# Performance work log

Measured on AMD Instinct MI355X. Metric: run time of the kernel, lower is better.

## Reference

```python
import jax, jax.numpy as jnp
import numpy as np


def _quant(x):
    # Per-tensor dynamic uint8 quantization to produce LUT row/col indices.
    # (The CUDA kernel's exact requant scheme is not in the source; this is the
    # assumed scheme: scale so max |x| -> 255, round, clip to [0,255].)
    s = 255.0 / jnp.maximum(jnp.max(jnp.abs(x)), jnp.float32(1e-6))
    return jnp.clip(jnp.round(x * s), 0, 255).astype(jnp.int32)


def _lut_conv(x, w, b, lut):
    # CustomAnyConv2d: stride=1, padding=(2,2), kernel 5x5.
    O, Cin, kh, kw = w.shape
    # im2col patches: (B, Cin*kh*kw, H, W), feature ordering matches w.reshape(O, -1)
    patches = jax.lax.conv_general_dilated_patches(
        x, (kh, kw), (1, 1), ((2, 2), (2, 2)))
    B, K, H, W = patches.shape
    pi = _quant(patches).reshape(B, K, H * W)            # (B,K,P)
    wi = _quant(w.reshape(O, K))                          # (O,K)
    vals = lut[pi[:, None, :, :], wi[None, :, :, None]]   # (B,O,K,P) gather
    out = vals.sum(axis=2).reshape(B, O, H, W)            # accumulate LUT products
    return out + b[None, :, None, None]


def _lut_dense(x, w, b, lut):
    # CustomAnyDense: out[h, o] = sum_k LUT[x[h,k], w[o,k]] + b[o]
    xi = _quant(x)                                        # (B,K)
    wi = _quant(w)                                        # (O,K)
    vals = lut[xi[:, None, :], wi[None, :, :]]            # (B,O,K)
    return vals.sum(axis=2) + b


def _maxpool2(x, pad=0):
    return jax.lax.reduce_window(
        x, -jnp.inf, jax.lax.max,
        (1, 1, 2, 2), (1, 1, 2, 2),
        ((0, 0), (0, 0), (pad, pad), (pad, pad)))


def setup_inputs() -> dict:
    key = jax.random.key(0)
    ks = jax.random.split(key, 11)
    B = 32
    x = jax.random.uniform(ks[0], (B, 1, 28, 28), jnp.float32)
    ij = np.arange(256)
    # Approximate-multiplier LUT: high byte of exact 8x8-bit product (uint8-valued).
    lut = jnp.asarray(((ij[:, None] * ij[None, :]) >> 8).astype(np.float32))
    return {
        "x": x,
        "lut": lut,
        "w1": jax.random.uniform(ks[1], (16, 1, 5, 5), jnp.float32),
        "b1": jax.random.normal(ks[2], (16,), jnp.float32) * 0.01,
        "w2": jax.random.uniform(ks[3], (32, 16, 5, 5), jnp.float32),
        "b2": jax.random.normal(ks[4], (32,), jnp.float32) * 0.01,
        "w3": jax.random.uniform(ks[5], (64, 32, 5, 5), jnp.float32),
        "b3": jax.random.normal(ks[6], (64,), jnp.float32) * 0.01,
        "fw1": jax.random.uniform(ks[7], (256, 1024), jnp.float32),
        "fb1": jax.random.normal(ks[8], (256,), jnp.float32) * 0.01,
        "fw2": jax.random.uniform(ks[9], (10, 256), jnp.float32),
        "fb2": jax.random.normal(ks[10], (10,), jnp.float32) * 0.01,
    }


def reference(x, lut, w1, b1, w2, b2, w3, b3, fw1, fb1, fw2, fb2):
    h = jax.nn.relu(_lut_conv(x, w1, b1, lut))
    h = _maxpool2(h)                     # (B,16,14,14)
    h = jax.nn.relu(_lut_conv(h, w2, b2, lut))
    h = _maxpool2(h)                     # (B,32,7,7)
    h = jax.nn.relu(_lut_conv(h, w3, b3, lut))
    h = _maxpool2(h, pad=1)              # (B,64,4,4)
    h = h.reshape(h.shape[0], -1)        # (B,1024)
    h = jax.nn.relu(_lut_dense(h, fw1, fb1, lut))
    h = _lut_dense(h, fw2, fb2, lut)     # (B,10)
    return jax.nn.log_softmax(h, axis=1)
```

## Files before the change

### kernel.cpp

```cpp
#include <hip/hip_runtime.h>
#include <math.h>

typedef unsigned int  u32;
typedef unsigned short u16;
typedef unsigned short u16x2 __attribute__((ext_vector_type(2)));

#define MAGIC 0x5A17D0E5u

#define O_XFLAGS 256
#define O_FLAGS  1024
#define O_A1     4096
#define O_A2     405504
#define O_A3     606208
#define O_A4     737280

__device__ __forceinline__ float blk_max(float v, float* red) {
  int t = threadIdx.x;
  __syncthreads();
  red[t] = v;
  __syncthreads();
#pragma unroll
  for (int s = 128; s > 0; s >>= 1) {
    if (t < s) red[t] = fmaxf(red[t], red[t + s]);
    __syncthreads();
  }
  return red[0];
}

__device__ __forceinline__ void amax_f(float* slot, float v) {
  atomicMax((int*)slot, (int)__float_as_uint(v));
}

__device__ __forceinline__ u16 quant1(float v, float s) {
  float q = rintf(v * s);
  q = fminf(fmaxf(q, 0.0f), 255.0f);
  return (u16)q;
}

__device__ __forceinline__ void mac_u32(u32& acc, u32 a, u32 w) {
  u16x2 av = __builtin_bit_cast(u16x2, a);
  u16x2 wv = __builtin_bit_cast(u16x2, w);
  u16x2 p  = av * wv;
  acc += (__builtin_bit_cast(u32, p) >> 8) & 0x00FF00FFu;
}
__device__ __forceinline__ void mac4(u32& acc, uint4 a, uint4 w) {
  mac_u32(acc, a.x, w.x); mac_u32(acc, a.y, w.y);
  mac_u32(acc, a.z, w.z); mac_u32(acc, a.w, w.w);
}

__device__ __forceinline__ float fmax4(float4 v) {
  return fmaxf(fmaxf(fabsf(v.x), fabsf(v.y)), fmaxf(fabsf(v.z), fabsf(v.w)));
}

__global__ __launch_bounds__(256, 2) void k_conv1(
    const float* __restrict__ x, const float* __restrict__ w1, const float* __restrict__ b1,
    const float* __restrict__ w2, const float* __restrict__ w3,
    const float* __restrict__ fw1, const float* __restrict__ fw2,
    float* __restrict__ a1, float* wsf, u32* xflags) {
  __shared__ float sxf[1024];
  __shared__ unsigned char sx[1024];
  __shared__ u16 sw[64];
  __shared__ float red[256];
  const int t = threadIdx.x, bid = blockIdx.x;

  if (bid >= 256) {
    int sb = bid - 256;
    if (sb < 16) {
      const float4* x4 = (const float4*)x;
      float m = 0.f;
      for (int i = sb * 256 + t; i < 6272; i += 16 * 256) m = fmaxf(m, fmax4(x4[i]));
      m = blk_max(m, red);
      if (t == 0) {
        amax_f(wsf + 0, m);
        __hip_atomic_store(&xflags[sb], MAGIC, __ATOMIC_RELEASE, __HIP_MEMORY_SCOPE_AGENT);
      }
      return;
    }
    sb -= 16;
    const float* p; int n4, base, nb, slot;
    if (sb < 2)       { p = w2;  n4 = 3200;  base = sb;      nb = 2;  slot = 2; }
    else if (sb < 10) { p = w3;  n4 = 12800; base = sb - 2;  nb = 8;  slot = 3; }
    else if (sb < 58) { p = fw1; n4 = 65536; base = sb - 10; nb = 48; slot = 4; }
    else              { p = fw2; n4 = 640;   base = 0;       nb = 1;  slot = 5; }
    const float4* p4 = (const float4*)p;
    float m = 0.f;
    for (int i = base * 256 + t; i < n4; i += nb * 256) m = fmaxf(m, fmax4(p4[i]));
    m = blk_max(m, red);
    if (t == 0) amax_f(wsf + slot, m);
    return;
  }

  int b = bid >> 3, op = bid & 7;
  float m = 0.f;
  if (t < 100) m = fmax4(((const float4*)w1)[t]);
  float w1max = blk_max(m, red);
  float sw1s = 255.0f / fmaxf(w1max, 1e-6f);
  for (int i = t; i < 1024; i += 256) sxf[i] = 0.f;
  __syncthreads();
  for (int i = t; i < 784; i += 256) {
    int y = i / 28, xx = i - y * 28;
    sxf[(y + 2) * 32 + xx + 2] = x[b * 784 + i];
  }
  if (t < 50) sw[t] = quant1(w1[op * 50 + t], sw1s);
  {
    int it = 0, ok = 0;
    do {
      u32 f = (t < 16) ? __hip_atomic_load(&xflags[t], __ATOMIC_RELAXED, __HIP_MEMORY_SCOPE_AGENT)
                       : MAGIC;
      ok = __syncthreads_and(f == MAGIC);
      if (!ok) __builtin_amdgcn_s_sleep(1);
    } while (!ok && ++it < 2000000);
    __threadfence();
  }
  float s0 = 255.0f / fmaxf(wsf[0], 1e-6f);
  for (int i = t; i < 1024; i += 256) sx[i] = (unsigned char)quant1(sxf[i], s0);
  __syncthreads();
  float lm = 0.f;
  if (t < 196) {
    int py = t / 14, px = t - py * 14;
#pragma unroll
    for (int ol = 0; ol < 2; ++ol) {
      int oc = op * 2 + ol;
      int best = -2147483647;
#pragma unroll
      for (int dy = 0; dy < 2; ++dy)
#pragma unroll
        for (int dx = 0; dx < 2; ++dx) {
          int cy = 2 * py + dy, cx = 2 * px + dx;
          int acc = 0;
#pragma unroll
          for (int kh = 0; kh < 5; ++kh) {
            const unsigned char* xp = sx + (cy + kh) * 32 + cx;
#pragma unroll
            for (int kw = 0; kw < 5; ++kw)
              acc += ((int)xp[kw] * (int)sw[ol * 25 + kh * 5 + kw]) >> 8;
          }
          best = max(best, acc);
        }
      float v = fmaxf(0.f, (float)best + b1[oc]);
      a1[b * 3136 + t * 16 + oc] = v;
      lm = fmaxf(lm, v);
    }
  }
  lm = blk_max(lm, red);
  if (t == 0) amax_f(wsf + 6, lm);
}

__global__ __launch_bounds__(256) void k_conv2(
    const float* __restrict__ a1, const float* __restrict__ w2, const float* __restrict__ b2,
    float* __restrict__ a2, float* wsf) {
  __shared__ __align__(16) u16 sa[324 * 16];
  __shared__ __align__(16) u16 sw[800];
  __shared__ int sconv[196];
  __shared__ float red[256];
  const int t = threadIdx.x, bid = blockIdx.x;
  int b = bid >> 4, og = bid & 15;
  float s1 = 255.0f / fmaxf(wsf[6], 1e-6f);
  float sw2 = 255.0f / fmaxf(wsf[2], 1e-6f);
  u32* sz = (u32*)sa;
  for (int i = t; i < 2592; i += 256) sz[i] = 0;
  __syncthreads();
  for (int i = t; i < 3136; i += 256) {
    int px = i >> 4, c = i & 15;
    int y = px / 14, xx = px - y * 14;
    sa[((y + 2) * 18 + xx + 2) * 16 + c] = quant1(a1[b * 3136 + i], s1);
  }
  for (int i = t; i < 800; i += 256) {
    int ol = i / 400, r = i - ol * 400, c = r / 25, tp = r - c * 25;
    sw[ol * 400 + tp * 16 + c] = quant1(w2[(og * 2 + ol) * 400 + c * 25 + tp], sw2);
  }
  __syncthreads();
  int h = t & 1, pxb = t >> 1;
  float lm = 0.f;
  for (int ol = 0; ol < 2; ++ol) {
    int oc = og * 2 + ol;
    const uint4* wq = (const uint4*)(sw + ol * 400);
#pragma unroll
    for (int rep = 0; rep < 2; ++rep) {
      int px = pxb + rep * 128;
      if (px < 196) {
        int y = px / 14, xx = px - y * 14;
        u32 acc = 0;
#pragma unroll
        for (int kh = 0; kh < 5; ++kh)
#pragma unroll
          for (int kw = 0; kw < 5; ++kw) {
            int row = (y + kh) * 18 + (xx + kw);
            uint4 av = *(const uint4*)(sa + row * 16 + h * 8);
            mac4(acc, av, wq[(kh * 5 + kw) * 2 + h]);
          }
        int ai = (int)((acc & 0xFFFFu) + (acc >> 16));
        ai += __shfl_down(ai, 1, 2);
        if (h == 0) sconv[px] = ai;
      }
    }
    __syncthreads();
    if (t < 49) {
      int py = t / 7, px = t - py * 7;
      int mm = sconv[(2 * py) * 14 + 2 * px];
      mm = max(mm, sconv[(2 * py) * 14 + 2 * px + 1]);
      mm = max(mm, sconv[(2 * py + 1) * 14 + 2 * px]);
      mm = max(mm, sconv[(2 * py + 1) * 14 + 2 * px + 1]);
      float v = fmaxf(0.f, (float)mm + b2[oc]);
      a2[b * 1568 + t * 32 + oc] = v;
      lm = fmaxf(lm, v);
    }
    __syncthreads();
  }
  lm = blk_max(lm, red);
  if (t == 0) amax_f(wsf + 7, lm);
}

__global__ __launch_bounds__(256) void k_conv3(
    const float* __restrict__ a2, const float* __restrict__ w3, const float* __restrict__ b3,
    float* __restrict__ a3, float* wsf) {
  __shared__ __align__(16) u16 sa[121 * 40];
  __shared__ __align__(16) u16 sw[4 * 800];
  __shared__ float red[256];
  const int t = threadIdx.x, bid = blockIdx.x;
  int b = bid >> 4, og = bid & 15;
  float s2 = 255.0f / fmaxf(wsf[7], 1e-6f);
  float sw3 = 255.0f / fmaxf(wsf[3], 1e-6f);
  u32* sz = (u32*)sa;
  for (int i = t; i < 2420; i += 256) sz[i] = 0;
  __syncthreads();
  for (int i = t; i < 1568; i += 256) {
    int px = i >> 5, c = i & 31;
    int y = px / 7, xx = px - y * 7;
    sa[((y + 2) * 11 + xx + 2) * 40 + c] = quant1(a2[b * 1568 + i], s2);
  }
  for (int i = t; i < 3200; i += 256) {
    int ol = i / 800, r = i - ol * 800, c = r / 25, tp = r - c * 25;
    sw[ol * 800 + tp * 32 + c] = quant1(w3[(og * 4 + ol) * 800 + c * 25 + tp], sw3);
  }
  __syncthreads();
  int q = t & 3, pos = t >> 2;
  int dydx = pos & 3, r = pos >> 2;
  int py = r >> 2, px = r & 3;
  int cy = 2 * py - 1 + (dydx >> 1), cx = 2 * px - 1 + (dydx & 1);
  bool valid = (cy >= 0 && cy < 7 && cx >= 0 && cx < 7);
  float lm = 0.f;
  for (int ol = 0; ol < 4; ++ol) {
    int oc = og * 4 + ol;
    int ai = 0;
    if (valid) {
      u32 acc = 0;
#pragma unroll
      for (int kh = 0; kh < 5; ++kh)
#pragma unroll
        for (int kw = 0; kw < 5; ++kw) {
          int row = (cy + kh) * 11 + (cx + kw);
          uint4 av = *(const uint4*)(sa + row * 40 + q * 8);
          uint4 wv = *(const uint4*)(sw + ol * 800 + (kh * 5 + kw) * 32 + q * 8);
          mac4(acc, av, wv);
        }
      ai = (int)((acc & 0xFFFFu) + (acc >> 16));
    }
    ai += __shfl_down(ai, 2, 4);
    ai += __shfl_down(ai, 1, 4);
    int val = valid ? ai : -(1 << 30);
    int mm = max(val, __shfl_down(val, 4, 16));
    mm = max(mm, __shfl_down(mm, 8, 16));
    if ((t & 15) == 0) {
      float v = fmaxf(0.f, (float)mm + b3[oc]);
      a3[b * 1024 + oc * 16 + r] = v;
      lm = fmaxf(lm, v);
    }
  }
  lm = blk_max(lm, red);
  if (t == 0) amax_f(wsf + 8, lm);
}

__global__ __launch_bounds__(256) void k_dense12(
    const float* __restrict__ a3f, const float* __restrict__ fw1, const float* __restrict__ fb1,
    const float* __restrict__ fw2, const float* __restrict__ fb2,
    float* __restrict__ a4, float* __restrict__ out, float* wsf, u32* flags) {
  __shared__ union {
    struct { u16 sh[1024]; } p;
    struct { u16 sh2[32 * 264]; u16 qw[2560]; float zb[320]; } w;
  } sm;
  __shared__ float red[256];
  const int t = threadIdx.x, bid = blockIdx.x;

  if (bid < 512) {
    int b = bid >> 4, og = bid & 15;
    float s3 = 255.0f / fmaxf(wsf[8], 1e-6f);
    float sws = 255.0f / fmaxf(wsf[4], 1e-6f);
    for (int i = t; i < 1024; i += 256)
      sm.p.sh[i] = quant1(a3f[b * 1024 + i], s3);
    __syncthreads();
    int ol = t >> 4, ks = t & 15;
    int o = og * 16 + ol;
    const float4* wf = (const float4*)(fw1 + o * 1024);
    const uint4* hp = (const uint4*)sm.p.sh;
    u32 acc = 0;
#pragma unroll
    for (int j = 0; j < 8; ++j) {
      int e = j * 16 + ks;
      float4 f0 = wf[e * 2], f1 = wf[e * 2 + 1];
      uint4 wv;
      wv.x = (u32)quant1(f0.x, sws) | ((u32)quant1(f0.y, sws) << 16);
      wv.y = (u32)quant1(f0.z, sws) | ((u32)quant1(f0.w, sws) << 16);
      wv.z = (u32)quant1(f1.x, sws) | ((u32)quant1(f1.y, sws) << 16);
      wv.w = (u32)quant1(f1.z, sws) | ((u32)quant1(f1.w, sws) << 16);
      mac4(acc, hp[e], wv);
    }
    int ai = (int)((acc & 0xFFFFu) + (acc >> 16));
#pragma unroll
    for (int d = 8; d > 0; d >>= 1)
      ai += __shfl_down(ai, d, 16);
    float lm = 0.f;
    if (ks == 0) {
      float v = fmaxf(0.f, (float)ai + fb1[o]);
      a4[b * 256 + o] = v;
      lm = v;
    }
    lm = blk_max(lm, red);
    if (t == 0) amax_f(wsf + 9, lm);
    __syncthreads();
    if (t == 0)
      __hip_atomic_store(&flags[bid], MAGIC, __ATOMIC_RELEASE, __HIP_MEMORY_SCOPE_AGENT);
    return;
  }

  {
    long it = 0;
    int ok = 0;
    do {
      u32 f1 = __hip_atomic_load(&flags[t],       __ATOMIC_RELAXED, __HIP_MEMORY_SCOPE_AGENT);
      u32 f2 = __hip_atomic_load(&flags[t + 256], __ATOMIC_RELAXED, __HIP_MEMORY_SCOPE_AGENT);
      ok = __syncthreads_and((f1 == MAGIC) && (f2 == MAGIC));
      if (!ok) __builtin_amdgcn_s_sleep(1);
    } while (!ok && ++it < 4000000);
    __threadfence();
  }
  float s4 = 255.0f / fmaxf(wsf[9], 1e-6f);
  float s5 = 255.0f / fmaxf(wsf[5], 1e-6f);
  for (int i = t; i < 8192; i += 256) {
    int b = i >> 8, k = i & 255;
    sm.w.sh2[b * 264 + k] = quant1(a4[i], s4);
  }
  for (int i = t; i < 2560; i += 256) sm.w.qw[i] = quant1(fw2[i], s5);
  __syncthreads();
  for (int task = t; task < 320; task += 256) {
    int b = task / 10, o = task - b * 10;
    const uint4* wp = (const uint4*)(sm.w.qw + o * 256);
    const uint4* hp = (const uint4*)(sm.w.sh2 + b * 264);
    u32 acc = 0;
#pragma unroll
    for (int j = 0; j < 32; ++j)
      mac4(acc, hp[j], wp[j]);
    sm.w.zb[task] = (float)((acc & 0xFFFFu) + (acc >> 16)) + fb2[o];
  }
  __syncthreads();
  for (int task = t; task < 320; task += 256) {
    int b = task / 10;
    const float* z = sm.w.zb + b * 10;
    float m = z[0];
#pragma unroll
    for (int j = 1; j < 10; ++j) m = fmaxf(m, z[j]);
    float se = 0.f;
#pragma unroll
    for (int j = 0; j < 10; ++j) se += expf(z[j] - m);
    out[task] = sm.w.zb[task] - (m + logf(se));
  }
}

extern "C" void kernel_launch(void* const* d_in, const int* in_sizes, int n_in,
                              void* d_out, int out_size, void* d_ws, size_t ws_size,
                              hipStream_t stream) {
  const float* x   = (const float*)d_in[0];
  const float* w1  = (const float*)d_in[2];
  const float* b1  = (const float*)d_in[3];
  const float* w2  = (const float*)d_in[4];
  const float* b2  = (const float*)d_in[5];
  const float* w3  = (const float*)d_in[6];
  const float* b3  = (const float*)d_in[7];
  const float* fw1 = (const float*)d_in[8];
  const float* fb1 = (const float*)d_in[9];
  const float* fw2 = (const float*)d_in[10];
  const float* fb2 = (const float*)d_in[11];
  float* out = (float*)d_out;
  unsigned char* ws8 = (unsigned char*)d_ws;
  float* wsf = (float*)d_ws;
  u32* xflags = (u32*)(ws8 + O_XFLAGS);
  u32* flags  = (u32*)(ws8 + O_FLAGS);
  float* A1 = (float*)(ws8 + O_A1);
  float* A2 = (float*)(ws8 + O_A2);
  float* A3 = (float*)(ws8 + O_A3);
  float* A4 = (float*)(ws8 + O_A4);

  k_conv1  <<<331, 256, 0, stream>>>(x, w1, b1, w2, w3, fw1, fw2, A1, wsf, xflags);
  k_conv2  <<<512, 256, 0, stream>>>(A1, w2, b2, A2, wsf);
  k_conv3  <<<512, 256, 0, stream>>>(A2, w3, b3, A3, wsf);
  k_dense12<<<513, 256, 0, stream>>>(A3, fw1, fb1, fw2, fb2, A4, out, wsf, flags);
}
```

Before: 158.5 us.

## Replace inter-block spin-wait flags with redundant reductions and a separate dense2 launch

Conv1 no longer waits on flag blocks that compute the global input max. Every conv block now recomputes the full input abs-max itself, quantizes straight into byte shared memory, and the 2-launch-bound hint is dropped. The fused dense kernel, which spun on 512 flags before its final block ran, is split into two kernels. Dense2 now uses 32 small blocks, one per batch row, instead of a single block. This removes spin-wait latency and the serial tail block, at the cost of redundant global reads of x in each block and one more kernel launch.

```diff
diff --git a/kernel.cpp b/kernel.cpp
--- a/kernel.cpp
+++ b/kernel.cpp
@@ -5,10 +5,6 @@
 typedef unsigned short u16;
 typedef unsigned short u16x2 __attribute__((ext_vector_type(2)));
 
-#define MAGIC 0x5A17D0E5u
-
-#define O_XFLAGS 256
-#define O_FLAGS  1024
 #define O_A1     4096
 #define O_A2     405504
 #define O_A3     606208
@@ -52,12 +48,11 @@
   return fmaxf(fmaxf(fabsf(v.x), fabsf(v.y)), fmaxf(fabsf(v.z), fabsf(v.w)));
 }
 
-__global__ __launch_bounds__(256, 2) void k_conv1(
+__global__ __launch_bounds__(256) void k_conv1(
     const float* __restrict__ x, const float* __restrict__ w1, const float* __restrict__ b1,
     const float* __restrict__ w2, const float* __restrict__ w3,
     const float* __restrict__ fw1, const float* __restrict__ fw2,
-    float* __restrict__ a1, float* wsf, u32* xflags) {
-  __shared__ float sxf[1024];
+    float* __restrict__ a1, float* wsf) {
   __shared__ unsigned char sx[1024];
   __shared__ u16 sw[64];
   __shared__ float red[256];
@@ -65,18 +60,6 @@
 
   if (bid >= 256) {
     int sb = bid - 256;
-    if (sb < 16) {
-      const float4* x4 = (const float4*)x;
-      float m = 0.f;
-      for (int i = sb * 256 + t; i < 6272; i += 16 * 256) m = fmaxf(m, fmax4(x4[i]));
-      m = blk_max(m, red);
-      if (t == 0) {
-        amax_f(wsf + 0, m);
-        __hip_atomic_store(&xflags[sb], MAGIC, __ATOMIC_RELEASE, __HIP_MEMORY_SCOPE_AGENT);
-      }
-      return;
-    }
-    sb -= 16;
     const float* p; int n4, base, nb, slot;
     if (sb < 2)       { p = w2;  n4 = 3200;  base = sb;      nb = 2;  slot = 2; }
     else if (sb < 10) { p = w3;  n4 = 12800; base = sb - 2;  nb = 8;  slot = 3; }
@@ -92,28 +75,23 @@
 
   int b = bid >> 3, op = bid & 7;
   float m = 0.f;
+  const float4* x4 = (const float4*)x;
+  for (int i = t; i < 6272; i += 256) m = fmaxf(m, fmax4(x4[i]));
+  float xmax = blk_max(m, red);
+  m = 0.f;
   if (t < 100) m = fmax4(((const float4*)w1)[t]);
   float w1max = blk_max(m, red);
-  float sw1s = 255.0f / fmaxf(w1max, 1e-6f);
-  for (int i = t; i < 1024; i += 256) sxf[i] = 0.f;
+  float s0  = 255.0f / fmaxf(xmax, 1e-6f);
+  float sw1 = 255.0f / fmaxf(w1max, 1e-6f);
+
+  u32* sxz = (u32*)sx;
+  for (int i = t; i < 256; i += 256) sxz[i] = 0;
   __syncthreads();
   for (int i = t; i < 784; i += 256) {
     int y = i / 28, xx = i - y * 28;
-    sxf[(y + 2) * 32 + xx + 2] = x[b * 784 + i];
-  }
-  if (t < 50) sw[t] = quant1(w1[op * 50 + t], sw1s);
-  {
-    int it = 0, ok = 0;
-    do {
-      u32 f = (t < 16) ? __hip_atomic_load(&xflags[t], __ATOMIC_RELAXED, __HIP_MEMORY_SCOPE_AGENT)
-                       : MAGIC;
-      ok = __syncthreads_and(f == MAGIC);
-      if (!ok) __builtin_amdgcn_s_sleep(1);
-    } while (!ok && ++it < 2000000);
-    __threadfence();
-  }
-  float s0 = 255.0f / fmaxf(wsf[0], 1e-6f);
-  for (int i = t; i < 1024; i += 256) sx[i] = (unsigned char)quant1(sxf[i], s0);
+    sx[(y + 2) * 32 + xx + 2] = (unsigned char)quant1(x[b * 784 + i], s0);
+  }
+  if (t < 50) sw[t] = quant1(w1[op * 50 + t], sw1);
   __syncthreads();
   float lm = 0.f;
   if (t < 196) {
@@ -271,32 +249,68 @@
   if (t == 0) amax_f(wsf + 8, lm);
 }
 
-__global__ __launch_bounds__(256) void k_dense12(
+__global__ __launch_bounds__(256) void k_dense1(
     const float* __restrict__ a3f, const float* __restrict__ fw1, const float* __restrict__ fb1,
-    const float* __restrict__ fw2, const float* __restrict__ fb2,
-    float* __restrict__ a4, float* __restrict__ out, float* wsf, u32* flags) {
-  __shared__ union {
-    struct { u16 sh[1024]; } p;
-    struct { u16 sh2[32 * 264]; u16 qw[2560]; float zb[320]; } w;
-  } sm;
+    float* __restrict__ a4, float* wsf) {
+  __shared__ __align__(16) u16 sh[1024];
   __shared__ float red[256];
   const int t = threadIdx.x, bid = blockIdx.x;
-
-  if (bid < 512) {
-    int b = bid >> 4, og = bid & 15;
-    float s3 = 255.0f / fmaxf(wsf[8], 1e-6f);
-    float sws = 255.0f / fmaxf(wsf[4], 1e-6f);
-    for (int i = t; i < 1024; i += 256)
-      sm.p.sh[i] = quant1(a3f[b * 1024 + i], s3);
-    __syncthreads();
-    int ol = t >> 4, ks = t & 15;
-    int o = og * 16 + ol;
-    const float4* wf = (const float4*)(fw1 + o * 1024);
-    const uint4* hp = (const uint4*)sm.p.sh;
+  int b = bid >> 4, og = bid & 15;
+  float s3 = 255.0f / fmaxf(wsf[8], 1e-6f);
+  float sws = 255.0f / fmaxf(wsf[4], 1e-6f);
+  for (int i = t; i < 1024; i += 256)
+    sh[i] = quant1(a3f[b * 1024 + i], s3);
+  __syncthreads();
+  int ol = t >> 4, ks = t & 15;
+  int o = og * 16 + ol;
+  const float4* wf = (const float4*)(fw1 + o * 1024);
+  const uint4* hp = (const uint4*)sh;
+  u32 acc = 0;
+#pragma unroll
+  for (int j = 0; j < 8; ++j) {
+    int e = j * 16 + ks;
+    float4 f0 = wf[e * 2], f1 = wf[e * 2 + 1];
+    uint4 wv;
+    wv.x = (u32)quant1(f0.x, sws) | ((u32)quant1(f0.y, sws) << 16);
+    wv.y = (u32)quant1(f0.z, sws) | ((u32)quant1(f0.w, sws) << 16);
+    wv.z = (u32)quant1(f1.x, sws) | ((u32)quant1(f1.y, sws) << 16);
+    wv.w = (u32)quant1(f1.z, sws) | ((u32)quant1(f1.w, sws) << 16);
+    mac4(acc, hp[e], wv);
+  }
+  int ai = (int)((acc & 0xFFFFu) + (acc >> 16));
+#pragma unroll
+  for (int d = 8; d > 0; d >>= 1)
+    ai += __shfl_down(ai, d, 16);
+  float lm = 0.f;
+  if (ks == 0) {
+    float v = fmaxf(0.f, (float)ai + fb1[o]);
+    a4[b * 256 + o] = v;
+    lm = v;
+  }
+  lm = blk_max(lm, red);
+  if (t == 0) amax_f(wsf + 9, lm);
+}
+
+__global__ __launch_bounds__(64) void k_dense2(
+    const float* __restrict__ a4, const float* __restrict__ fw2, const float* __restrict__ fb2,
+    float* __restrict__ out, float* wsf) {
+  int b = blockIdx.x;
+  __shared__ __align__(16) u16 sh[256];
+  __shared__ float z[16];
+  int t = threadIdx.x;
+  float s4 = 255.0f / fmaxf(wsf[9], 1e-6f);
+  float sws = 255.0f / fmaxf(wsf[5], 1e-6f);
+  for (int i = t; i < 256; i += 64)
+    sh[i] = quant1(a4[b * 256 + i], s4);
+  __syncthreads();
+  if (t < 40) {
+    int o = t >> 2, ks = t & 3;
+    const float4* wf = (const float4*)(fw2 + o * 256);
+    const uint4* hp = (const uint4*)sh;
     u32 acc = 0;
 #pragma unroll
     for (int j = 0; j < 8; ++j) {
-      int e = j * 16 + ks;
+      int e = j * 4 + ks;
       float4 f0 = wf[e * 2], f1 = wf[e * 2 + 1];
       uint4 wv;
       wv.x = (u32)quant1(f0.x, sws) | ((u32)quant1(f0.y, sws) << 16);
@@ -306,63 +320,19 @@
       mac4(acc, hp[e], wv);
     }
     int ai = (int)((acc & 0xFFFFu) + (acc >> 16));
-#pragma unroll
-    for (int d = 8; d > 0; d >>= 1)
-      ai += __shfl_down(ai, d, 16);
-    float lm = 0.f;
-    if (ks == 0) {
-      float v = fmaxf(0.f, (float)ai + fb1[o]);
-      a4[b * 256 + o] = v;
-      lm = v;
-    }
-    lm = blk_max(lm, red);
-    if (t == 0) amax_f(wsf + 9, lm);
-    __syncthreads();
-    if (t == 0)
-      __hip_atomic_store(&flags[bid], MAGIC, __ATOMIC_RELEASE, __HIP_MEMORY_SCOPE_AGENT);
-    return;
-  }
-
-  {
-    long it = 0;
-    int ok = 0;
-    do {
-      u32 f1 = __hip_atomic_load(&flags[t],       __ATOMIC_RELAXED, __HIP_MEMORY_SCOPE_AGENT);
-      u32 f2 = __hip_atomic_load(&flags[t + 256], __ATOMIC_RELAXED, __HIP_MEMORY_SCOPE_AGENT);
-      ok = __syncthreads_and((f1 == MAGIC) && (f2 == MAGIC));
-      if (!ok) __builtin_amdgcn_s_sleep(1);
-    } while (!ok && ++it < 4000000);
-    __threadfence();
-  }
-  float s4 = 255.0f / fmaxf(wsf[9], 1e-6f);
-  float s5 = 255.0f / fmaxf(wsf[5], 1e-6f);
-  for (int i = t; i < 8192; i += 256) {
-    int b = i >> 8, k = i & 255;
-    sm.w.sh2[b * 264 + k] = quant1(a4[i], s4);
-  }
-  for (int i = t; i < 2560; i += 256) sm.w.qw[i] = quant1(fw2[i], s5);
-  __syncthreads();
-  for (int task = t; task < 320; task += 256) {
-    int b = task / 10, o = task - b * 10;
-    const uint4* wp = (const uint4*)(sm.w.qw + o * 256);
-    const uint4* hp = (const uint4*)(sm.w.sh2 + b * 264);
-    u32 acc = 0;
-#pragma unroll
-    for (int j = 0; j < 32; ++j)
-      mac4(acc, hp[j], wp[j]);
-    sm.w.zb[task] = (float)((acc & 0xFFFFu) + (acc >> 16)) + fb2[o];
-  }
-  __syncthreads();
-  for (int task = t; task < 320; task += 256) {
-    int b = task / 10;
-    const float* z = sm.w.zb + b * 10;
+    ai += __shfl_down(ai, 2, 4);
+    ai += __shfl_down(ai, 1, 4);
+    if (ks == 0) z[o] = (float)ai + fb2[o];
+  }
+  __syncthreads();
+  if (t < 10) {
     float m = z[0];
 #pragma unroll
     for (int j = 1; j < 10; ++j) m = fmaxf(m, z[j]);
     float se = 0.f;
 #pragma unroll
     for (int j = 0; j < 10; ++j) se += expf(z[j] - m);
-    out[task] = sm.w.zb[task] - (m + logf(se));
+    out[b * 10 + t] = z[t] - (m + logf(se));
   }
 }
 
@@ -383,15 +353,14 @@
   float* out = (float*)d_out;
   unsigned char* ws8 = (unsigned char*)d_ws;
   float* wsf = (float*)d_ws;
-  u32* xflags = (u32*)(ws8 + O_XFLAGS);
-  u32* flags  = (u32*)(ws8 + O_FLAGS);
   float* A1 = (float*)(ws8 + O_A1);
   float* A2 = (float*)(ws8 + O_A2);
   float* A3 = (float*)(ws8 + O_A3);
   float* A4 = (float*)(ws8 + O_A4);
 
-  k_conv1  <<<331, 256, 0, stream>>>(x, w1, b1, w2, w3, fw1, fw2, A1, wsf, xflags);
-  k_conv2  <<<512, 256, 0, stream>>>(A1, w2, b2, A2, wsf);
-  k_conv3  <<<512, 256, 0, stream>>>(A2, w3, b3, A3, wsf);
-  k_dense12<<<513, 256, 0, stream>>>(A3, fw1, fb1, fw2, fb2, A4, out, wsf, flags);
-}
+  k_conv1 <<<315, 256, 0, stream>>>(x, w1, b1, w2, w3, fw1, fw2, A1, wsf);
+  k_conv2 <<<512, 256, 0, stream>>>(A1, w2, b2, A2, wsf);
+  k_conv3 <<<512, 256, 0, stream>>>(A2, w3, b3, A3, wsf);
+  k_dense1<<<512, 256, 0, stream>>>(A3, fw1, fb1, A4, wsf);
+  k_dense2<<<32, 64, 0, stream>>>(A4, fw2, fb2, out, wsf);
+}
```

After: 142.3 us. 1.11x faster.
